# Kernel tuning notes

Measured on AMD Instinct MI355X. Metric: run time of the kernel, lower is better.

The kernel has to match this reference:

```python
import jax, jax.numpy as jnp
import numpy as np

B = 8192          # batch of scenes
H = 20            # human_num
O = 10            # other_robot_num
IN = 13           # input_dim
SELF = 6          # self_state_dim
AG = IN - SELF    # agent_state_dim = 7
E1, E2 = 256, 128 # wr_dims / wh_dims
HID = 32          # hardcoded hidden_channels in Graphgnn
FIN = 128         # final_state_dim
P1, P2, P3 = 256, 128, 1  # planning_dims
NE = 8            # number of hetero edge types
# edge-type index convention:
# 0 robot->human, 1 human->robot, 2 other->robot, 3 robot->other,
# 4 other->human, 5 human->other, 6 human->human, 7 other->other


def setup_inputs() -> dict:
    key = jax.random.key(0)
    ks = iter(jax.random.split(key, 40))
    def nrm(shape, scale=0.05):
        return jax.random.normal(next(ks), shape, jnp.float32) * scale
    inp = {}
    inp["state"] = jax.random.normal(next(ks), (B, H + O, IN), jnp.float32)
    inp["dropout"] = 0  # unused by forward (kept for signature fidelity)
    # w_r: SELF -> E1 -> E2 (last_relu=True)
    inp["wr_W0"] = nrm((SELF, E1)); inp["wr_b0"] = nrm((E1,))
    inp["wr_W1"] = nrm((E1, E2));   inp["wr_b1"] = nrm((E2,))
    # w_h: AG -> E1 -> E2
    inp["wh_W0"] = nrm((AG, E1));   inp["wh_b0"] = nrm((E1,))
    inp["wh_W1"] = nrm((E1, E2));   inp["wh_b1"] = nrm((E2,))
    # w_o: AG -> E1 -> E2
    inp["wo_W0"] = nrm((AG, E1));   inp["wo_b0"] = nrm((E1,))
    inp["wo_W1"] = nrm((E1, E2));   inp["wo_b1"] = nrm((E2,))
    # per-edge-type GraphConv params (PyG GraphConv: lin_rel has bias, lin_root has none)
    inp["c1_relW"]  = nrm((NE, E2, HID)); inp["c1_relb"]  = nrm((NE, HID))
    inp["c1_rootW"] = nrm((NE, E2, HID))
    inp["c2_relW"]  = nrm((NE, HID, FIN)); inp["c2_relb"]  = nrm((NE, FIN))
    inp["c2_rootW"] = nrm((NE, HID, FIN))
    # value_net: FIN -> P1 -> P2 -> P3 (no final relu)
    inp["v_W0"] = nrm((FIN, P1)); inp["v_b0"] = nrm((P1,))
    inp["v_W1"] = nrm((P1, P2));  inp["v_b1"] = nrm((P2,))
    inp["v_W2"] = nrm((P2, P3));  inp["v_b2"] = nrm((P3,))
    return inp


def _mlp2(x, W0, b0, W1, b1, last_relu):
    h = jax.nn.relu(x @ W0 + b0)
    h = h @ W1 + b1
    return jax.nn.relu(h) if last_relu else h


def _hetero_conv(xr, xh, xo, relW, relb, rootW):
    # xr: [B,1,D], xh: [B,H,D], xo: [B,O,D]
    # GraphConv per edge type: out_dst = lin_root(x_dst) + lin_rel(sum of src messages)
    # graph is complete bipartite (sence) / complete-minus-self (affect),
    # so aggregations are closed-form sums.
    lin  = lambda x, i: jnp.einsum('bnd,do->bno', x, relW[i]) + relb[i]
    root = lambda x, i: jnp.einsum('bnd,do->bno', x, rootW[i])
    sh = xh.sum(axis=1, keepdims=True)  # [B,1,D] sum over humans
    so = xo.sum(axis=1, keepdims=True)  # [B,1,D] sum over other robots
    # robot receives: human->robot (1), other->robot (2)
    out_r = lin(sh, 1) + root(xr, 1) + lin(so, 2) + root(xr, 2)
    # human receives: robot->human (0), other->human (4), human->human (6)
    out_h = (lin(xr, 0) + root(xh, 0)
             + lin(so, 4) + root(xh, 4)
             + lin(sh - xh, 6) + root(xh, 6))
    # other receives: robot->other (3), human->other (5), other->other (7)
    out_o = (lin(xr, 3) + root(xo, 3)
             + lin(sh, 5) + root(xo, 5)
             + lin(so - xo, 7) + root(xo, 7))
    return out_r, out_h, out_o


def reference(state, dropout,
              wr_W0, wr_b0, wr_W1, wr_b1,
              wh_W0, wh_b0, wh_W1, wh_b1,
              wo_W0, wo_b0, wo_W1, wo_b1,
              c1_relW, c1_relb, c1_rootW,
              c2_relW, c2_relb, c2_rootW,
              v_W0, v_b0, v_W1, v_b1, v_W2, v_b2):
    self_state = state[:, 0, :SELF]          # [B, SELF]
    human_states = state[:, :H, SELF:]       # [B, H, AG]
    other_states = state[:, H:, SELF:]       # [B, O, AG]
    er = _mlp2(self_state, wr_W0, wr_b0, wr_W1, wr_b1, True)[:, None, :]  # [B,1,E2]
    eh = _mlp2(human_states, wh_W0, wh_b0, wh_W1, wh_b1, True)            # [B,H,E2]
    eo = _mlp2(other_states, wo_W0, wo_b0, wo_W1, wo_b1, True)            # [B,O,E2]
    r, h, o = _hetero_conv(er, eh, eo, c1_relW, c1_relb, c1_rootW)
    r, h, o = jax.nn.relu(r), jax.nn.relu(h), jax.nn.relu(o)
    r, h, o = _hetero_conv(r, h, o, c2_relW, c2_relb, c2_rootW)
    r = jax.nn.relu(r)
    hr = r[:, 0, :]                           # robot node per scene, [B, FIN]
    v = jax.nn.relu(hr @ v_W0 + v_b0)
    v = jax.nn.relu(v @ v_W1 + v_b1)
    v = v @ v_W2 + v_b2                       # [B, 1]
    return v
```

## Files before the change

kernel.cpp:

```cpp
#include <hip/hip_runtime.h>
#include <hip/hip_bf16.h>
#include <stdint.h>

#define BATCH 8192
#define NSTATE 30
#define DIN 13
#define E1 256
#define E2 128

typedef short bf16x8 __attribute__((ext_vector_type(8)));
typedef float f32x4 __attribute__((ext_vector_type(4)));

__device__ __forceinline__ unsigned short f2b(float f) {
    unsigned u = __float_as_uint(f);
    u += 0x7FFFu + ((u >> 16) & 1u);
    return (unsigned short)(u >> 16);
}
__device__ __forceinline__ float b2f(unsigned short b) {
    return __uint_as_float((unsigned)b << 16);
}
__device__ __forceinline__ unsigned pack2(float a, float b) {
    return ((unsigned)f2b(fmaxf(b, 0.f)) << 16) | f2b(fmaxf(a, 0.f));
}
__device__ __forceinline__ unsigned pack2n(float a, float b) {
    return ((unsigned)f2b(b) << 16) | f2b(a);
}

__device__ __forceinline__ float wcat_val(int k, int m, const float* relW, const float* rootW) {
    int part = k >> 7, c = k & 127, grp = m >> 5, mm = m & 31;
    int off = c * 32 + mm;
    if (part == 0) return (grp == 0) ? rootW[4096 + off] + rootW[8192 + off]
                        : (grp == 1) ? relW[off] : relW[3*4096 + off];
    if (part == 1) return (grp == 0) ? relW[1*4096 + off]
                        : (grp == 1) ? relW[6*4096 + off] : relW[5*4096 + off];
    return (grp == 0) ? relW[2*4096 + off]
         : (grp == 1) ? relW[4*4096 + off] : relW[7*4096 + off];
}
__device__ __forceinline__ float wc2_val(int k, int n, const float* relW, const float* rootW) {
    int grp = k >> 5, kk = k & 31;
    int off = kk * 128 + n;
    if (grp == 0) return rootW[4096 + off] + rootW[8192 + off];
    if (grp == 1) return relW[4096 + off];
    return relW[8192 + off];
}

__global__ void k_prep(const float* __restrict__ c1_relW, const float* __restrict__ c1_relb,
                       const float* __restrict__ c1_rootW,
                       const float* __restrict__ c2_relW, const float* __restrict__ c2_relb,
                       const float* __restrict__ c2_rootW,
                       const float* __restrict__ wh_W0, const float* __restrict__ wh_W1,
                       const float* __restrict__ wo_W0, const float* __restrict__ wo_W1,
                       const float* __restrict__ wr_W0, const float* __restrict__ wr_W1,
                       const float* __restrict__ v_W0, const float* __restrict__ v_W1,
                       float* __restrict__ bcat, float* __restrict__ bc2,
                       unsigned short* __restrict__ W0b_h, unsigned short* __restrict__ W0b_o,
                       unsigned short* __restrict__ W0b_r,
                       unsigned short* __restrict__ W1f_h, unsigned short* __restrict__ W1f_o,
                       unsigned short* __restrict__ W1f_r,
                       unsigned short* __restrict__ Mf_h, unsigned short* __restrict__ Mf_o,
                       unsigned short* __restrict__ Wcatf, unsigned short* __restrict__ Wc2f,
                       unsigned short* __restrict__ vW0f, unsigned short* __restrict__ vW1f)
{
    int gid = blockIdx.x * blockDim.x + threadIdx.x;
    int gsz = gridDim.x * blockDim.x;

    for (int i = gid; i < 96; i += gsz) {
        int grp = i >> 5, mm = i & 31;
        float v;
        if (grp == 0)      v = c1_relb[32 + mm] + c1_relb[64 + mm];
        else if (grp == 1) v = c1_relb[mm] + c1_relb[128 + mm] + c1_relb[192 + mm];
        else               v = c1_relb[96 + mm] + c1_relb[160 + mm] + c1_relb[224 + mm];
        bcat[i] = v;
    }
    for (int i = gid; i < 128; i += gsz) bc2[i] = c2_relb[128 + i] + c2_relb[256 + i];

    for (int i = gid; i < 2048; i += gsz) {
        int n = i >> 3, j = i & 7;
        W0b_h[i] = (j < 7) ? f2b(wh_W0[j * 256 + n]) : 0;
        W0b_o[i] = (j < 7) ? f2b(wo_W0[j * 256 + n]) : 0;
        W0b_r[i] = (j < 6) ? f2b(wr_W0[j * 256 + n]) : 0;
    }
    for (int i = gid; i < 32768; i += gsz) {
        int j = i & 7, l = (i >> 3) & 63, nt = (i >> 9) & 7, ks = i >> 12;
        int k = ks * 32 + (l >> 4) * 8 + j;
        int n = nt * 16 + (l & 15);
        W1f_h[i] = f2b(wh_W1[k * 128 + n]);
        W1f_o[i] = f2b(wo_W1[k * 128 + n]);
        W1f_r[i] = f2b(wr_W1[k * 128 + n]);
    }
    for (int i = gid; i < 4096; i += gsz) {
        int j = i & 7, l = (i >> 3) & 63, nt = (i >> 9) & 1, ks = i >> 10;
        int k = ks * 32 + (l >> 4) * 8 + j;
        int n = nt * 16 + (l & 15);
        int i0 = k * 32 + n;
        Mf_h[i] = f2b(c1_rootW[i0] + c1_rootW[4*4096 + i0] + c1_rootW[6*4096 + i0] - c1_relW[6*4096 + i0]);
        Mf_o[i] = f2b(c1_rootW[3*4096 + i0] + c1_rootW[5*4096 + i0] + c1_rootW[7*4096 + i0] - c1_relW[7*4096 + i0]);
    }
    for (int i = gid; i < 36864; i += gsz) {
        int j = i & 7, l = (i >> 3) & 63, rem = i >> 9;
        int nt = rem % 6, ks = rem / 6;
        int k = ks * 32 + (l >> 4) * 8 + j;
        int n = nt * 16 + (l & 15);
        Wcatf[i] = f2b(wcat_val(k, n, c1_relW, c1_rootW));
    }
    for (int i = gid; i < 12288; i += gsz) {
        int j = i & 7, l = (i >> 3) & 63, rem = i >> 9;
        int nt = rem & 7, ks = rem >> 3;
        int k = ks * 32 + (l >> 4) * 8 + j;
        int n = nt * 16 + (l & 15);
        Wc2f[i] = f2b(wc2_val(k, n, c2_relW, c2_rootW));
    }
    for (int i = gid; i < 32768; i += gsz) {
        int j = i & 7, l = (i >> 3) & 63, rem = i >> 9;
        int nt = rem & 15, ks = rem >> 4;
        int k = ks * 32 + (l >> 4) * 8 + j;
        int n = nt * 16 + (l & 15);
        vW0f[i] = f2b(v_W0[k * 256 + n]);
    }
    for (int i = gid; i < 32768; i += gsz) {
        int j = i & 7, l = (i >> 3) & 63, rem = i >> 9;
        int nt = rem & 7, ks = rem >> 3;
        int k = ks * 32 + (l >> 4) * 8 + j;
        int n = nt * 16 + (l & 15);
        vW1f[i] = f2b(v_W1[k * 128 + n]);
    }
}

#define SM_W0   0
#define SM_MF   4096
#define SM_W1   12288
#define SM_B0   77824
#define SM_B1   78848
#define SM_HS   79360
#define SM_SZ   (79360 + 8 * 16 * 264 * 2)

template<int NPB, int NODE0, int INOFF, int INDIM, bool TAIL>
__device__ __forceinline__ void mlp_blockE(
    int blkrow0, const float* __restrict__ state,
    const unsigned short* __restrict__ W0b_g, const float* __restrict__ b0,
    const unsigned short* __restrict__ W1f_g, const float* __restrict__ b1,
    const unsigned short* __restrict__ Mf_g,
    unsigned short* __restrict__ tR, float* __restrict__ sumB,
    unsigned short* __restrict__ eR, char* smem)
{
    unsigned short* W0s = (unsigned short*)(smem + SM_W0);
    unsigned short* Mfs = (unsigned short*)(smem + SM_MF);
    unsigned short* W1s = (unsigned short*)(smem + SM_W1);
    float* b0s          = (float*)(smem + SM_B0);
    float* b1s          = (float*)(smem + SM_B1);

    const int t = threadIdx.x;
    const int lane = t & 63;
    const int w = t >> 6;
    const int l15 = lane & 15;
    const int quad = lane >> 4;
    const int R0 = blkrow0 + w * 128;
    unsigned short* hw = (unsigned short*)(smem + SM_HS) + w * (16 * 264);
    unsigned short* ew = hw;

    if (t < 256) { ((uint4*)W0s)[t] = ((const uint4*)W0b_g)[t]; b0s[t] = b0[t]; }
    if (t >= 256 && t < 384) b1s[t - 256] = b1[t - 256];
    #pragma unroll
    for (int i = 0; i < 8; ++i)
        ((uint4*)W1s)[t + 512 * i] = ((const uint4*)W1f_g)[t + 512 * i];
    if constexpr (TAIL)
        ((uint4*)Mfs)[t] = ((const uint4*)Mf_g)[t];
    __syncthreads();

    float s0 = 0.f, s1 = 0.f;
    int bcur = R0 / NPB;

    for (int sub = 0; sub < 8; ++sub) {
        const int wrow0 = R0 + sub * 16;

        bf16x8 bx = {};
        if (quad == 0) {
            int grow = wrow0 + l15;
            int b = grow / NPB;
            int n = grow - b * NPB + NODE0;
            const float* xp = state + ((size_t)b * NSTATE + n) * DIN + INOFF;
            #pragma unroll
            for (int j = 0; j < INDIM; ++j)
                bx[j] = (short)f2b(xp[j]);
        }

        #pragma unroll
        for (int nt = 0; nt < 16; ++nt) {
            bf16x8 aw = {};
            if (quad == 0)
                aw = *(const bf16x8*)(W0s + (nt * 16 + l15) * 8);
            float4 bb = *(const float4*)(b0s + nt * 16 + quad * 4);
            f32x4 c = {bb.x, bb.y, bb.z, bb.w};
            c = __builtin_amdgcn_mfma_f32_16x16x32_bf16(aw, bx, c, 0, 0, 0);
            uint2 pv = {pack2(c[0], c[1]), pack2(c[2], c[3])};
            *(uint2*)(hw + l15 * 264 + nt * 16 + quad * 4) = pv;
        }

        f32x4 acc[8];
        #pragma unroll
        for (int nt = 0; nt < 8; ++nt) {
            float4 bb = *(const float4*)(b1s + nt * 16 + quad * 4);
            acc[nt] = (f32x4){bb.x, bb.y, bb.z, bb.w};
        }
        #pragma unroll
        for (int ks = 0; ks < 8; ++ks) {
            bf16x8 bh = *(const bf16x8*)(hw + l15 * 264 + ks * 32 + quad * 8);
            #pragma unroll
            for (int nt = 0; nt < 8; ++nt) {
                bf16x8 aw = *(const bf16x8*)(W1s + ((ks * 8 + nt) * 64 + lane) * 8);
                acc[nt] = __builtin_amdgcn_mfma_f32_16x16x32_bf16(aw, bh, acc[nt], 0, 0, 0);
            }
        }

        if constexpr (TAIL) {
            __asm__ __volatile__("s_waitcnt lgkmcnt(0)" ::: "memory");
            #pragma unroll
            for (int nt = 0; nt < 8; ++nt) {
                uint2 pv = {pack2(acc[nt][0], acc[nt][1]), pack2(acc[nt][2], acc[nt][3])};
                *(uint2*)(ew + l15 * 136 + nt * 16 + quad * 4) = pv;
            }

            f32x4 tacc[2] = {{0.f,0.f,0.f,0.f},{0.f,0.f,0.f,0.f}};
            #pragma unroll
            for (int ks = 0; ks < 4; ++ks) {
                bf16x8 ae = *(const bf16x8*)(ew + l15 * 136 + ks * 32 + quad * 8);
                #pragma unroll
                for (int nt = 0; nt < 2; ++nt) {
                    bf16x8 bm = *(const bf16x8*)(Mfs + ((ks * 2 + nt) * 64 + lane) * 8);
                    tacc[nt] = __builtin_amdgcn_mfma_f32_16x16x32_bf16(bm, ae, tacc[nt], 0, 0, 0);
                }
            }
            #pragma unroll
            for (int nt = 0; nt < 2; ++nt) {
                uint2 pv = {pack2n(tacc[nt][0], tacc[nt][1]), pack2n(tacc[nt][2], tacc[nt][3])};
                *(uint2*)(tR + (size_t)(wrow0 + l15) * 32 + nt * 16 + quad * 4) = pv;
            }

            #pragma unroll
            for (int r = 0; r < 16; ++r) {
                int b = (wrow0 + r) / NPB;
                if (b != bcur) {
                    bool interior = (bcur * NPB >= R0) && ((bcur + 1) * NPB <= R0 + 128);
                    float* dst = sumB + (size_t)bcur * 128 + 2 * lane;
                    if (interior) { dst[0] = s0; dst[1] = s1; }
                    else { atomicAdd(dst, s0); atomicAdd(dst + 1, s1); }
                    s0 = 0.f; s1 = 0.f; bcur = b;
                }
                unsigned v = *(const unsigned*)(ew + r * 136 + lane * 2);
                s0 += b2f((unsigned short)v);
                s1 += b2f((unsigned short)(v >> 16));
            }
            if (sub == 7) {
                bool interior = (bcur * NPB >= R0) && ((bcur + 1) * NPB <= R0 + 128);
                float* dst = sumB + (size_t)bcur * 128 + 2 * lane;
                if (interior) { dst[0] = s0; dst[1] = s1; }
                else { atomicAdd(dst, s0); atomicAdd(dst + 1, s1); }
            }
        } else {
            #pragma unroll
            for (int nt = 0; nt < 8; ++nt) {
                uint2 pv = {pack2(acc[nt][0], acc[nt][1]), pack2(acc[nt][2], acc[nt][3])};
                *(uint2*)(eR + (size_t)(wrow0 + l15) * 128 + nt * 16 + quad * 4) = pv;
            }
        }
        __asm__ __volatile__("" ::: "memory");
    }
}

__global__ __launch_bounds__(512, 2) void k_mlpE(
    const float* __restrict__ state,
    const unsigned short* __restrict__ W0b_h, const float* __restrict__ b0_h,
    const unsigned short* __restrict__ W1f_h, const float* __restrict__ b1_h,
    const unsigned short* __restrict__ Mf_h, unsigned short* __restrict__ tR_h,
    float* __restrict__ shB,
    const unsigned short* __restrict__ W0b_o, const float* __restrict__ b0_o,
    const unsigned short* __restrict__ W1f_o, const float* __restrict__ b1_o,
    const unsigned short* __restrict__ Mf_o, unsigned short* __restrict__ tR_o,
    float* __restrict__ soB,
    const unsigned short* __restrict__ W0b_r, const float* __restrict__ b0_r,
    const unsigned short* __restrict__ W1f_r, const float* __restrict__ b1_r,
    unsigned short* __restrict__ eR)
{
    __shared__ __align__(16) char smem[SM_SZ];
    int bid = blockIdx.x;
    if (bid < 160)
        mlp_blockE<20, 0, 6, 7, true>(bid * 1024, state, W0b_h, b0_h, W1f_h, b1_h,
                                      Mf_h, tR_h, shB, nullptr, smem);
    else if (bid < 240)
        mlp_blockE<10, 20, 6, 7, true>((bid - 160) * 1024, state, W0b_o, b0_o, W1f_o, b1_o,
                                       Mf_o, tR_o, soB, nullptr, smem);
    else
        mlp_blockE<1, 0, 0, 6, false>((bid - 240) * 1024, state, W0b_r, b0_r, W1f_r, b1_r,
                                      nullptr, nullptr, nullptr, eR, smem);
}

__global__ __launch_bounds__(256, 2) void k_tail(
    const unsigned short* __restrict__ eR,
    const float* __restrict__ shB, const float* __restrict__ soB,
    const unsigned short* __restrict__ tR_h, const unsigned short* __restrict__ tR_o,
    const unsigned short* __restrict__ Wcatf, const float* __restrict__ bcat,
    const unsigned short* __restrict__ Wc2f, const float* __restrict__ bc2,
    const unsigned short* __restrict__ vW0f, const float* __restrict__ vb0,
    const unsigned short* __restrict__ vW1f, const float* __restrict__ vb1,
    const float* __restrict__ vW2, const float* __restrict__ vb2,
    float* __restrict__ out)
{
    __shared__ __align__(16) char sm[33024];
    unsigned short* Ub  = (unsigned short*)(sm);
    unsigned short* V1b = (unsigned short*)(sm);
    unsigned short* Vb  = (unsigned short*)(sm + 12800);
    float* chL          = (float*)(sm + 16128);
    float* coL          = (float*)(sm + 18176);
    unsigned short* Hb  = (unsigned short*)(sm + 20224);
    float* V2b          = (float*)(sm + 24576);

    const int t = threadIdx.x, lane = t & 63, w = t >> 6;
    const int l15 = lane & 15, quad = lane >> 4;
    const int b0 = blockIdx.x * 16;
    const int rowb = quad * 4;

    {
        int b = t >> 4, q = t & 15;
        ((uint4*)(Ub + b * 400))[q] = ((const uint4*)(eR + (size_t)(b0 + b) * 128))[q];
    }
    for (int idx = t; idx < 4096; idx += 256) {
        int b = idx >> 8, kk = idx & 255;
        float v = (kk < 128) ? shB[(size_t)(b0 + b) * 128 + kk]
                             : soB[(size_t)(b0 + b) * 128 + kk - 128];
        Ub[b * 400 + 128 + kk] = f2b(v);
    }
    __syncthreads();

    for (int nt = w; nt < 6; nt += 4) {
        float bias = bcat[nt * 16 + l15];
        f32x4 acc = {bias, bias, bias, bias};
        #pragma unroll
        for (int ks = 0; ks < 12; ++ks) {
            bf16x8 a = *(const bf16x8*)(Ub + l15 * 400 + ks * 32 + quad * 8);
            bf16x8 bw = *(const bf16x8*)(Wcatf + ((ks * 6 + nt) * 64 + lane) * 8);
            acc = __builtin_amdgcn_mfma_f32_16x16x32_bf16(a, bw, acc, 0, 0, 0);
        }
        int n = nt * 16 + l15;
        #pragma unroll
        for (int reg = 0; reg < 4; ++reg) {
            float v = acc[reg];
            int b = rowb + reg;
            if (n < 32)      Vb[b * 104 + n] = f2b(fmaxf(v, 0.f));
            else if (n < 64) chL[b * 32 + (n - 32)] = v;
            else             coL[b * 32 + (n - 64)] = v;
        }
    }
    __syncthreads();

    for (int idx = t; idx < 512; idx += 256) {
        int b = idx >> 5, m = idx & 31;
        float ch = chL[b * 32 + m];
        const unsigned short* p = tR_h + (size_t)(b0 + b) * 20 * 32 + m;
        float s = 0.f;
        #pragma unroll
        for (int n = 0; n < 20; ++n) s += fmaxf(ch + b2f(p[n * 32]), 0.f);
        Vb[b * 104 + 32 + m] = f2b(s);
        float co = coL[b * 32 + m];
        const unsigned short* p2 = tR_o + (size_t)(b0 + b) * 10 * 32 + m;
        float s2 = 0.f;
        #pragma unroll
        for (int n = 0; n < 10; ++n) s2 += fmaxf(co + b2f(p2[n * 32]), 0.f);
        Vb[b * 104 + 64 + m] = f2b(s2);
    }
    __syncthreads();

    {
        f32x4 acc[2];
        #pragma unroll
        for (int q = 0; q < 2; ++q) {
            int nt = w + q * 4;
            float bias = bc2[nt * 16 + l15];
            acc[q] = (f32x4){bias, bias, bias, bias};
        }
        #pragma unroll
        for (int ks = 0; ks < 3; ++ks) {
            bf16x8 a = *(const bf16x8*)(Vb + l15 * 104 + ks * 32 + quad * 8);
            #pragma unroll
            for (int q = 0; q < 2; ++q) {
                int nt = w + q * 4;
                bf16x8 bw = *(const bf16x8*)(Wc2f + ((ks * 8 + nt) * 64 + lane) * 8);
                acc[q] = __builtin_amdgcn_mfma_f32_16x16x32_bf16(a, bw, acc[q], 0, 0, 0);
            }
        }
        #pragma unroll
        for (int q = 0; q < 2; ++q) {
            int nt = w + q * 4;
            #pragma unroll
            for (int reg = 0; reg < 4; ++reg)
                Hb[(rowb + reg) * 136 + nt * 16 + l15] = f2b(fmaxf(acc[q][reg], 0.f));
        }
    }
    __syncthreads();

    {
        f32x4 acc[4];
        #pragma unroll
        for (int q = 0; q < 4; ++q) {
            int nt = w + q * 4;
            float bias = vb0[nt * 16 + l15];
            acc[q] = (f32x4){bias, bias, bias, bias};
        }
        #pragma unroll
        for (int ks = 0; ks < 4; ++ks) {
            bf16x8 a = *(const bf16x8*)(Hb + l15 * 136 + ks * 32 + quad * 8);
            #pragma unroll
            for (int q = 0; q < 4; ++q) {
                int nt = w + q * 4;
                bf16x8 bw = *(const bf16x8*)(vW0f + ((ks * 16 + nt) * 64 + lane) * 8);
                acc[q] = __builtin_amdgcn_mfma_f32_16x16x32_bf16(a, bw, acc[q], 0, 0, 0);
            }
        }
        __syncthreads();
        #pragma unroll
        for (int q = 0; q < 4; ++q) {
            int nt = w + q * 4;
            #pragma unroll
            for (int reg = 0; reg < 4; ++reg)
                V1b[(rowb + reg) * 264 + nt * 16 + l15] = f2b(fmaxf(acc[q][reg], 0.f));
        }
    }
    __syncthreads();

    {
        f32x4 acc[2];
        #pragma unroll
        for (int q = 0; q < 2; ++q) {
            int nt = w + q * 4;
            float bias = vb1[nt * 16 + l15];
            acc[q] = (f32x4){bias, bias, bias, bias};
        }
        #pragma unroll
        for (int ks = 0; ks < 8; ++ks) {
            bf16x8 a = *(const bf16x8*)(V1b + l15 * 264 + ks * 32 + quad * 8);
            #pragma unroll
            for (int q = 0; q < 2; ++q) {
                int nt = w + q * 4;
                bf16x8 bw = *(const bf16x8*)(vW1f + ((ks * 8 + nt) * 64 + lane) * 8);
                acc[q] = __builtin_amdgcn_mfma_f32_16x16x32_bf16(a, bw, acc[q], 0, 0, 0);
            }
        }
        #pragma unroll
        for (int q = 0; q < 2; ++q) {
            int nt = w + q * 4;
            #pragma unroll
            for (int reg = 0; reg < 4; ++reg)
                V2b[(rowb + reg) * 132 + nt * 16 + l15] = fmaxf(acc[q][reg], 0.f);
        }
    }
    __syncthreads();

    if (t < 128) {
        int b = t >> 3, j = t & 7;
        float v = 0.f;
        #pragma unroll
        for (int k = 0; k < 16; ++k)
            v = fmaf(V2b[b * 132 + j * 16 + k], vW2[j * 16 + k], v);
        v += __shfl_down(v, 4, 8);
        v += __shfl_down(v, 2, 8);
        v += __shfl_down(v, 1, 8);
        if (j == 0) out[b0 + b] = v + vb2[0];
    }
}

extern "C" void kernel_launch(void* const* d_in, const int* in_sizes, int n_in,
                              void* d_out, int out_size, void* d_ws, size_t ws_size,
                              hipStream_t stream)
{
    const float* state   = (const float*)d_in[0];
    const float* wr_W0   = (const float*)d_in[2];
    const float* wr_b0   = (const float*)d_in[3];
    const float* wr_W1   = (const float*)d_in[4];
    const float* wr_b1   = (const float*)d_in[5];
    const float* wh_W0   = (const float*)d_in[6];
    const float* wh_b0   = (const float*)d_in[7];
    const float* wh_W1   = (const float*)d_in[8];
    const float* wh_b1   = (const float*)d_in[9];
    const float* wo_W0   = (const float*)d_in[10];
    const float* wo_b0   = (const float*)d_in[11];
    const float* wo_W1   = (const float*)d_in[12];
    const float* wo_b1   = (const float*)d_in[13];
    const float* c1_relW = (const float*)d_in[14];
    const float* c1_relb = (const float*)d_in[15];
    const float* c1_rootW= (const float*)d_in[16];
    const float* c2_relW = (const float*)d_in[17];
    const float* c2_relb = (const float*)d_in[18];
    const float* c2_rootW= (const float*)d_in[19];
    const float* v_W0    = (const float*)d_in[20];
    const float* v_b0    = (const float*)d_in[21];
    const float* v_W1    = (const float*)d_in[22];
    const float* v_b1    = (const float*)d_in[23];
    const float* v_W2    = (const float*)d_in[24];
    const float* v_b2    = (const float*)d_in[25];

    char* ws = (char*)d_ws;
    size_t off = 0;
    auto alloc = [&](size_t bytes) -> char* {
        char* p = ws + off;
        off = (off + bytes + 255) & ~(size_t)255;
        return p;
    };
    float* shB  = (float*)alloc((size_t)BATCH * 128 * 4);
    float* soB  = (float*)alloc((size_t)BATCH * 128 * 4);
    unsigned short* tR_h = (unsigned short*)alloc((size_t)163840 * 32 * 2);
    unsigned short* tR_o = (unsigned short*)alloc((size_t)81920 * 32 * 2);
    unsigned short* eR   = (unsigned short*)alloc((size_t)BATCH * 128 * 2);
    float* bcat = (float*)alloc(96 * 4);
    float* bc2  = (float*)alloc(128 * 4);
    unsigned short* W0b_h = (unsigned short*)alloc(2048 * 2);
    unsigned short* W0b_o = (unsigned short*)alloc(2048 * 2);
    unsigned short* W0b_r = (unsigned short*)alloc(2048 * 2);
    unsigned short* W1f_h = (unsigned short*)alloc(32768 * 2);
    unsigned short* W1f_o = (unsigned short*)alloc(32768 * 2);
    unsigned short* W1f_r = (unsigned short*)alloc(32768 * 2);
    unsigned short* Mf_h  = (unsigned short*)alloc(4096 * 2);
    unsigned short* Mf_o  = (unsigned short*)alloc(4096 * 2);
    unsigned short* Wcatf = (unsigned short*)alloc(36864 * 2);
    unsigned short* Wc2f  = (unsigned short*)alloc(12288 * 2);
    unsigned short* vW0f  = (unsigned short*)alloc(32768 * 2);
    unsigned short* vW1f  = (unsigned short*)alloc(32768 * 2);
    (void)ws_size; (void)in_sizes; (void)n_in; (void)out_size;

    hipMemsetAsync(shB, 0, (size_t)2 * BATCH * 128 * 4, stream);

    k_prep<<<256, 256, 0, stream>>>(c1_relW, c1_relb, c1_rootW, c2_relW, c2_relb, c2_rootW,
                                    wh_W0, wh_W1, wo_W0, wo_W1, wr_W0, wr_W1, v_W0, v_W1,
                                    bcat, bc2, W0b_h, W0b_o, W0b_r, W1f_h, W1f_o, W1f_r,
                                    Mf_h, Mf_o, Wcatf, Wc2f, vW0f, vW1f);

    k_mlpE<<<248, 512, 0, stream>>>(state,
                                    W0b_h, wh_b0, W1f_h, wh_b1, Mf_h, tR_h, shB,
                                    W0b_o, wo_b0, W1f_o, wo_b1, Mf_o, tR_o, soB,
                                    W0b_r, wr_b0, W1f_r, wr_b1, eR);

    k_tail<<<512, 256, 0, stream>>>(eR, shB, soB, tR_h, tR_o,
                                    Wcatf, bcat, Wc2f, bc2, vW0f, v_b0, vW1f, v_b1,
                                    v_W2, v_b2, (float*)d_out);
}
```

Before: 173.7 us.

## Hold half of W1 in registers, shrink LDS, fold zeroing into prep kernel

The MLP kernel now keeps the first half of the W1 fragment tiles (32 bf16x8 per lane) in VGPRs and stages only the second half in shared memory, cutting LDS use per block by 32 KB. This is meant to reduce LDS traffic in the inner MFMA loop and ease LDS capacity limits on residency. Separately, the hipMemsetAsync of the accumulation buffers is replaced by a zeroing loop inside k_prep, removing one stream operation. The register cache adds 128 VGPRs per thread, which under launch_bounds(512,2) risks spills or lower occupancy.

Result: no change. 176.2 us (+1.5%).

```diff
diff --git a/kernel.cpp b/kernel.cpp
--- a/kernel.cpp
+++ b/kernel.cpp
@@ -52,6 +52,7 @@
                        const float* __restrict__ wo_W0, const float* __restrict__ wo_W1,
                        const float* __restrict__ wr_W0, const float* __restrict__ wr_W1,
                        const float* __restrict__ v_W0, const float* __restrict__ v_W1,
+                       float* __restrict__ zeroBuf,
                        float* __restrict__ bcat, float* __restrict__ bc2,
                        unsigned short* __restrict__ W0b_h, unsigned short* __restrict__ W0b_o,
                        unsigned short* __restrict__ W0b_r,
@@ -64,6 +65,12 @@
     int gid = blockIdx.x * blockDim.x + threadIdx.x;
     int gsz = gridDim.x * blockDim.x;
 
+    {
+        float4 z = {0.f, 0.f, 0.f, 0.f};
+        for (int i = gid; i < 2 * BATCH * 128 / 4; i += gsz)
+            ((float4*)zeroBuf)[i] = z;
+    }
+
     for (int i = gid; i < 96; i += gsz) {
         int grp = i >> 5, mm = i & 31;
         float v;
@@ -129,13 +136,13 @@
 #define SM_W0   0
 #define SM_MF   4096
 #define SM_W1   12288
-#define SM_B0   77824
-#define SM_B1   78848
-#define SM_HS   79360
-#define SM_SZ   (79360 + 8 * 16 * 264 * 2)
+#define SM_B0   45056
+#define SM_B1   46080
+#define SM_HS   46592
+#define SM_SZ   (46592 + 8 * 16 * 264 * 2)
 
 template<int NPB, int NODE0, int INOFF, int INDIM, bool TAIL>
-__device__ __forceinline__ void mlp_blockE(
+__device__ __forceinline__ void mlp_blockF(
     int blkrow0, const float* __restrict__ state,
     const unsigned short* __restrict__ W0b_g, const float* __restrict__ b0,
     const unsigned short* __restrict__ W1f_g, const float* __restrict__ b1,
@@ -161,10 +168,16 @@
     if (t < 256) { ((uint4*)W0s)[t] = ((const uint4*)W0b_g)[t]; b0s[t] = b0[t]; }
     if (t >= 256 && t < 384) b1s[t - 256] = b1[t - 256];
     #pragma unroll
-    for (int i = 0; i < 8; ++i)
-        ((uint4*)W1s)[t + 512 * i] = ((const uint4*)W1f_g)[t + 512 * i];
+    for (int i = 0; i < 4; ++i)
+        ((uint4*)W1s)[t + 512 * i] = ((const uint4*)W1f_g)[2048 + t + 512 * i];
     if constexpr (TAIL)
         ((uint4*)Mfs)[t] = ((const uint4*)Mf_g)[t];
+
+    bf16x8 w1r[32];
+    #pragma unroll
+    for (int f = 0; f < 32; ++f)
+        w1r[f] = *(const bf16x8*)(W1f_g + ((size_t)f * 64 + lane) * 8);
+
     __syncthreads();
 
     float s0 = 0.f, s1 = 0.f;
@@ -207,7 +220,11 @@
             bf16x8 bh = *(const bf16x8*)(hw + l15 * 264 + ks * 32 + quad * 8);
             #pragma unroll
             for (int nt = 0; nt < 8; ++nt) {
-                bf16x8 aw = *(const bf16x8*)(W1s + ((ks * 8 + nt) * 64 + lane) * 8);
+                bf16x8 aw;
+                if (ks < 4)
+                    aw = w1r[ks * 8 + nt];
+                else
+                    aw = *(const bf16x8*)(W1s + (((ks - 4) * 8 + nt) * 64 + lane) * 8);
                 acc[nt] = __builtin_amdgcn_mfma_f32_16x16x32_bf16(aw, bh, acc[nt], 0, 0, 0);
             }
         }
@@ -267,7 +284,7 @@
     }
 }
 
-__global__ __launch_bounds__(512, 2) void k_mlpE(
+__global__ __launch_bounds__(512, 2) void k_mlpF(
     const float* __restrict__ state,
     const unsigned short* __restrict__ W0b_h, const float* __restrict__ b0_h,
     const unsigned short* __restrict__ W1f_h, const float* __restrict__ b1_h,
@@ -284,13 +301,13 @@
     __shared__ __align__(16) char smem[SM_SZ];
     int bid = blockIdx.x;
     if (bid < 160)
-        mlp_blockE<20, 0, 6, 7, true>(bid * 1024, state, W0b_h, b0_h, W1f_h, b1_h,
+        mlp_blockF<20, 0, 6, 7, true>(bid * 1024, state, W0b_h, b0_h, W1f_h, b1_h,
                                       Mf_h, tR_h, shB, nullptr, smem);
     else if (bid < 240)
-        mlp_blockE<10, 20, 6, 7, true>((bid - 160) * 1024, state, W0b_o, b0_o, W1f_o, b1_o,
+        mlp_blockF<10, 20, 6, 7, true>((bid - 160) * 1024, state, W0b_o, b0_o, W1f_o, b1_o,
                                        Mf_o, tR_o, soB, nullptr, smem);
     else
-        mlp_blockE<1, 0, 0, 6, false>((bid - 240) * 1024, state, W0b_r, b0_r, W1f_r, b1_r,
+        mlp_blockF<1, 0, 0, 6, false>((bid - 240) * 1024, state, W0b_r, b0_r, W1f_r, b1_r,
                                       nullptr, nullptr, nullptr, eR, smem);
 }
 
@@ -525,14 +542,13 @@
     unsigned short* vW1f  = (unsigned short*)alloc(32768 * 2);
     (void)ws_size; (void)in_sizes; (void)n_in; (void)out_size;
 
-    hipMemsetAsync(shB, 0, (size_t)2 * BATCH * 128 * 4, stream);
-
     k_prep<<<256, 256, 0, stream>>>(c1_relW, c1_relb, c1_rootW, c2_relW, c2_relb, c2_rootW,
                                     wh_W0, wh_W1, wo_W0, wo_W1, wr_W0, wr_W1, v_W0, v_W1,
+                                    shB,
                                     bcat, bc2, W0b_h, W0b_o, W0b_r, W1f_h, W1f_o, W1f_r,
                                     Mf_h, Mf_o, Wcatf, Wc2f, vW0f, vW1f);
 
-    k_mlpE<<<248, 512, 0, stream>>>(state,
+    k_mlpF<<<248, 512, 0, stream>>>(state,
                                     W0b_h, wh_b0, W1f_h, wh_b1, Mf_h, tR_h, shB,
                                     W0b_o, wo_b0, W1f_o, wo_b1, Mf_o, tR_o, soB,
                                     W0b_r, wr_b0, W1f_r, wr_b1, eR);
```
